# Optimization experiments

Measured on AMD Instinct MI355X. Metric: run time of the kernel, lower is better.

The kernel has to match this reference:

```python
import jax, jax.numpy as jnp
import numpy as np

HIDDEN = 2048
NUM_HEADS = 16
HEAD_DIM = HIDDEN // NUM_HEADS


def setup_inputs() -> dict:
    key = jax.random.key(0)
    k1, k2, k3 = jax.random.split(key, 3)
    B, S = 2, 2048
    hidden_states = jax.random.normal(k1, (B, S, HIDDEN), dtype=jnp.float32)
    attention_mask = jnp.zeros((B, 1, 1, S), dtype=jnp.float32)
    W_qkv = jax.random.normal(k2, (HIDDEN, 3 * HIDDEN), dtype=jnp.float32) * (1.0 / np.sqrt(HIDDEN))
    b_qkv = jnp.zeros((3 * HIDDEN,), dtype=jnp.float32)
    W_out = jax.random.normal(k3, (HIDDEN, HIDDEN), dtype=jnp.float32) * (1.0 / np.sqrt(HIDDEN))
    b_out = jnp.zeros((HIDDEN,), dtype=jnp.float32)
    return {"hidden_states": hidden_states, "attention_mask": attention_mask,
            "W_qkv": W_qkv, "b_qkv": b_qkv, "W_out": W_out, "b_out": b_out}


def reference(hidden_states, attention_mask, W_qkv, b_qkv, W_out, b_out):
    B, S, H = hidden_states.shape
    scale = 1.0 / np.sqrt(HEAD_DIM)
    # fused QKV projection (column-parallel linear, world_size=1)
    mixed = hidden_states @ W_qkv + b_qkv                      # [B,S,3H]
    q, k, v = jnp.split(mixed, 3, axis=-1)
    # [B, heads, S, head_dim]
    q = q.reshape(B, S, NUM_HEADS, HEAD_DIM).transpose(0, 2, 1, 3)
    k = k.reshape(B, S, NUM_HEADS, HEAD_DIM).transpose(0, 2, 1, 3)
    v = v.reshape(B, S, NUM_HEADS, HEAD_DIM).transpose(0, 2, 1, 3)
    scores = jnp.einsum('bhqd,bhkd->bhqk', q, k) * scale       # [B,h,S,S]
    scores = scores + attention_mask                            # additive mask broadcast
    probs = jax.nn.softmax(scores, axis=-1)
    ctx = jnp.einsum('bhqk,bhkd->bhqd', probs, v)               # [B,h,S,d]
    ctx = ctx.transpose(0, 2, 1, 3).reshape(B, S, H)
    return ctx @ W_out + b_out
```

## Files before the change

### kernel.cpp

```cpp
#include <hip/hip_runtime.h>
#include <hip/hip_bf16.h>
#include <stdint.h>

typedef __attribute__((ext_vector_type(4))) float   f32x4;
typedef __attribute__((ext_vector_type(8))) __bf16  bf16x8;
typedef __attribute__((ext_vector_type(4))) __bf16  bf16x4;
typedef __attribute__((ext_vector_type(8))) short   s16x8;
typedef __attribute__((ext_vector_type(4))) unsigned short u16x4;
typedef __attribute__((ext_vector_type(4))) float   fl4;

#define DEVFN static __device__ __forceinline__

constexpr int BATCH = 2, SEQ = 2048, HID = 2048, NHEAD = 16, HDIM = 128;
constexpr int MROWS = BATCH * SEQ;
constexpr int N3    = 3 * HID;
constexpr float ATT_SCALE = 0.08838834764831845f;
constexpr float LOG2E = 1.44269504088896340736f;

DEVFN unsigned short f2bf(float f) {
  unsigned int u = __float_as_uint(f);
  u += 0x7FFFu + ((u >> 16) & 1u);
  return (unsigned short)(u >> 16);
}
DEVFN float bf2f(unsigned short h) { return __uint_as_float(((unsigned int)h) << 16); }

DEVFN void async_cp16(const void* g, void* l) {
  __builtin_amdgcn_global_load_lds(
      (__attribute__((address_space(1))) void*)g,
      (__attribute__((address_space(3))) void*)l, 16, 0, 0);
}

DEVFN f32x4 mfma_bf16(bf16x8 a, bf16x8 b, f32x4 c) {
  return __builtin_amdgcn_mfma_f32_16x16x32_bf16(a, b, c, 0, 0, 0);
}

__global__ __launch_bounds__(256) void cvt_bf16(const float* __restrict__ x,
                                                unsigned short* __restrict__ hi, int n4) {
  for (int i = blockIdx.x * blockDim.x + threadIdx.x; i < n4; i += gridDim.x * blockDim.x) {
    fl4 v = ((const fl4*)x)[i];
    u16x4 h;
#pragma unroll
    for (int j = 0; j < 4; j++) h[j] = f2bf(v[j]);
    ((u16x4*)hi)[i] = h;
  }
}

__global__ __launch_bounds__(256) void cvt_transpose(const float* __restrict__ W,
                                                     unsigned short* __restrict__ T,
                                                     int R, int C) {
  __shared__ float tile[32][33];
  const int c0 = blockIdx.x * 32, r0 = blockIdx.y * 32;
  const int tx = threadIdx.x, ty = threadIdx.y;
#pragma unroll
  for (int i = 0; i < 4; i++) tile[ty + 8 * i][tx] = W[(size_t)(r0 + ty + 8 * i) * C + c0 + tx];
  __syncthreads();
#pragma unroll
  for (int i = 0; i < 4; i++) {
    const float v = tile[tx][ty + 8 * i];
    T[(size_t)(c0 + ty + 8 * i) * R + r0 + tx] = f2bf(v);
  }
}

template <bool OUT_BF16>
__global__ __launch_bounds__(256) void gemm_bt(const unsigned short* __restrict__ A,
                                               const unsigned short* __restrict__ Bt,
                                               const float* __restrict__ bias,
                                               void* __restrict__ Cout, int Ndim, int Kdim) {
  __shared__ __align__(16) unsigned short smem[2 * 128 * 64];
  unsigned short* sA = smem;
  unsigned short* sB = smem + 128 * 64;

  const int tid = threadIdx.x;
  const int wid = tid >> 6, lane = tid & 63;
  const int wm = wid >> 1, wn = wid & 1;
  const int g = lane >> 4, q = lane & 15;
  const int n0 = blockIdx.x * 128, m0 = blockIdx.y * 128;
  const int lrow = lane >> 3, lcolB = (lane & 7) << 4;

  f32x4 acc[4][4] = {};

  for (int k0 = 0; k0 < Kdim; k0 += 64) {
    __syncthreads();
#pragma unroll
    for (int i = 0; i < 4; i++) {
      const int trow = (wid << 5) + (i << 3) + lrow;
      const int scol = lcolB ^ ((trow & 7) << 4);
      const int dstB = ((wid << 5) + (i << 3)) << 7;
      async_cp16((const char*)A  + (((size_t)(m0 + trow) * Kdim + k0) << 1) + scol, (char*)sA + dstB);
      async_cp16((const char*)Bt + (((size_t)(n0 + trow) * Kdim + k0) << 1) + scol, (char*)sB + dstB);
    }
    __syncthreads();
#pragma unroll
    for (int kk = 0; kk < 2; kk++) {
      const int kbyte = (kk << 6) + (g << 4);
      bf16x8 a_h[4], b_h[4];
#pragma unroll
      for (int mf = 0; mf < 4; mf++) {
        const int row = (wm << 6) + (mf << 4) + q;
        a_h[mf] = *(const bf16x8*)((const char*)sA + (row << 7) + (kbyte ^ ((row & 7) << 4)));
      }
#pragma unroll
      for (int nf = 0; nf < 4; nf++) {
        const int row = (wn << 6) + (nf << 4) + q;
        b_h[nf] = *(const bf16x8*)((const char*)sB + (row << 7) + (kbyte ^ ((row & 7) << 4)));
      }
#pragma unroll
      for (int mf = 0; mf < 4; mf++)
#pragma unroll
        for (int nf = 0; nf < 4; nf++)
          acc[mf][nf] = mfma_bf16(a_h[mf], b_h[nf], acc[mf][nf]);
    }
  }

  float bv[4];
#pragma unroll
  for (int nf = 0; nf < 4; nf++) bv[nf] = bias[n0 + (wn << 6) + (nf << 4) + q];
#pragma unroll
  for (int mf = 0; mf < 4; mf++) {
    const int rowg = m0 + (wm << 6) + (mf << 4) + (g << 2);
#pragma unroll
    for (int nf = 0; nf < 4; nf++) {
      const int colg = n0 + (wn << 6) + (nf << 4) + q;
#pragma unroll
      for (int r = 0; r < 4; r++) {
        const float v = acc[mf][nf][r] + bv[nf];
        if (OUT_BF16)
          ((unsigned short*)Cout)[(size_t)(rowg + r) * Ndim + colg] = f2bf(v);
        else
          ((float*)Cout)[(size_t)(rowg + r) * Ndim + colg] = v;
      }
    }
  }
}

__global__ __launch_bounds__(256) void transpose_v(const unsigned short* __restrict__ qkv,
                                                   unsigned short* __restrict__ vt) {
  __shared__ __align__(16) unsigned short tile[64][136];
  const int z = blockIdx.y, b = z >> 4, h = z & 15;
  const int s0 = blockIdx.x << 6;
  const int t = threadIdx.x;
#pragma unroll
  for (int i = 0; i < 4; i++) {
    const int idx = t + (i << 8);
    const int row = idx >> 4, ch = idx & 15;
    *(s16x8*)&tile[row][ch << 3] =
        *(const s16x8*)(qkv + (size_t)(b * SEQ + s0 + row) * N3 + 2 * HID + h * HDIM + (ch << 3));
  }
  __syncthreads();
#pragma unroll
  for (int i = 0; i < 4; i++) {
    const int idx = t + (i << 8);
    const int d = idx >> 3, sc = idx & 7;
    s16x8 v;
#pragma unroll
    for (int j = 0; j < 8; j++) v[j] = (short)tile[(sc << 3) + j][d];
    *(s16x8*)(vt + (size_t)(z * HDIM + d) * SEQ + s0 + (sc << 3)) = v;
  }
}

__global__ __launch_bounds__(256, 2) void attn_kernel(const unsigned short* __restrict__ qkv,
                                                      const unsigned short* __restrict__ vt,
                                                      const float* __restrict__ mask,
                                                      unsigned short* __restrict__ ctx) {
  __shared__ __align__(16) unsigned short sK[64 * 128];
  __shared__ __align__(16) unsigned short sV[128 * 64];
  __shared__ __align__(16) unsigned short sP[4][32 * 72];

  const int z = blockIdx.y, b = z >> 4, h = z & 15;
  const int qb = blockIdx.x;
  const int tid = threadIdx.x, wid = tid >> 6, lane = tid & 63;
  const int g = lane >> 4, q = lane & 15;
  const int q0 = (qb << 7) + (wid << 5);

  bf16x8 bq[2][4];
#pragma unroll
  for (int qs = 0; qs < 2; qs++) {
    const unsigned short* qrow = qkv + (size_t)(b * SEQ + q0 + (qs << 4) + q) * N3 + h * HDIM;
#pragma unroll
    for (int c = 0; c < 4; c++) bq[qs][c] = *(const bf16x8*)(qrow + (c << 5) + (g << 3));
  }

  f32x4 acc[2][8] = {};
  float mrun[2] = {-1e30f, -1e30f}, lrun[2] = {0.f, 0.f};
  const int lrow8 = lane >> 3, lcol8 = (lane & 7) << 4;
  const int lrow16 = lane >> 4, lcol16 = (lane & 15) << 4;
  unsigned short* myP = &sP[wid][0];
  const int sbase = (lane & 48) | (g << 2);

  for (int k0 = 0; k0 < SEQ; k0 += 64) {
    __syncthreads();
#pragma unroll
    for (int i = 0; i < 4; i++) {
      const int kr = (wid << 4) + (i << 2) + lrow16;
      const int kcol = lcol16 ^ ((kr & 7) << 4);
      async_cp16((const char*)qkv + (((size_t)(b * SEQ + k0 + kr) * N3 + HID + h * HDIM) << 1) + kcol,
                 (char*)sK + (((wid << 4) + (i << 2)) << 8));
      const int vr = (wid << 5) + (i << 3) + lrow8;
      const int vcol = lcol8 ^ ((vr & 7) << 4);
      async_cp16((const char*)vt + (((size_t)(z * HDIM + vr) * SEQ + k0) << 1) + vcol,
                 (char*)sV + (((wid << 5) + (i << 3)) << 7));
    }
    __syncthreads();

    f32x4 accs[2][4];
#pragma unroll
    for (int qs = 0; qs < 2; qs++)
#pragma unroll
      for (int kt = 0; kt < 4; kt++) accs[qs][kt] = (f32x4){0.f, 0.f, 0.f, 0.f};
#pragma unroll
    for (int c = 0; c < 4; c++) {
      const int kbyte = (c << 6) + (g << 4);
#pragma unroll
      for (int kt = 0; kt < 4; kt++) {
        const int key = (kt << 4) + q;
        const bf16x8 ak = *(const bf16x8*)((const char*)sK + (key << 8) + (kbyte ^ ((key & 7) << 4)));
        accs[0][kt] = mfma_bf16(ak, bq[0][c], accs[0][kt]);
        accs[1][kt] = mfma_bf16(ak, bq[1][c], accs[1][kt]);
      }
    }

#pragma unroll
    for (int qs = 0; qs < 2; qs++) {
      float sv[4][4];
      float mt = -1e30f;
#pragma unroll
      for (int kt = 0; kt < 4; kt++) {
        const fl4 mk = *(const fl4*)(mask + (size_t)b * SEQ + k0 + (kt << 4) + (g << 2));
#pragma unroll
        for (int r = 0; r < 4; r++) {
          const float s = accs[qs][kt][r] * ATT_SCALE + mk[r];
          sv[kt][r] = s;
          mt = fmaxf(mt, s);
        }
      }
      mt = fmaxf(mt, __shfl_xor(mt, 16));
      mt = fmaxf(mt, __shfl_xor(mt, 32));
      if (!__all(mt <= mrun[qs] + 8.f)) {
        const float mnew = fmaxf(mrun[qs], mt);
        const float fs = exp2f((mrun[qs] - mnew) * LOG2E);
        lrun[qs] *= fs;
#pragma unroll
        for (int r = 0; r < 4; r++) {
          const float fr = __shfl(fs, sbase + r);
#pragma unroll
          for (int dt = 0; dt < 8; dt++) acc[qs][dt][r] *= fr;
        }
        mrun[qs] = mnew;
      }
      float ps = 0.f;
#pragma unroll
      for (int kt = 0; kt < 4; kt++) {
        bf16x4 pk;
#pragma unroll
        for (int r = 0; r < 4; r++) {
          const float e = exp2f((sv[kt][r] - mrun[qs]) * LOG2E);
          ps += e;
          pk[r] = (__bf16)e;
        }
        *(bf16x4*)((char*)myP + ((qs << 4) + q) * 144 + (((kt << 4) + (g << 2)) << 1)) = pk;
      }
      ps += __shfl_xor(ps, 16);
      ps += __shfl_xor(ps, 32);
      lrun[qs] += ps;
    }

    asm volatile("s_waitcnt lgkmcnt(0)" ::: "memory");
    __builtin_amdgcn_sched_barrier(0);

#pragma unroll
    for (int kc = 0; kc < 2; kc++) {
      const bf16x8 pa0 = *(const bf16x8*)((const char*)myP + q * 144 + (kc << 6) + (g << 4));
      const bf16x8 pa1 = *(const bf16x8*)((const char*)myP + (16 + q) * 144 + (kc << 6) + (g << 4));
      const int kbyte = (kc << 6) + (g << 4);
#pragma unroll
      for (int dt = 0; dt < 8; dt++) {
        const int d = (dt << 4) + q;
        const bf16x8 bvv = *(const bf16x8*)((const char*)sV + (d << 7) + (kbyte ^ ((d & 7) << 4)));
        acc[0][dt] = mfma_bf16(pa0, bvv, acc[0][dt]);
        acc[1][dt] = mfma_bf16(pa1, bvv, acc[1][dt]);
      }
    }
  }

#pragma unroll
  for (int qs = 0; qs < 2; qs++)
#pragma unroll
    for (int r = 0; r < 4; r++) {
      const float lr = __shfl(lrun[qs], sbase + r);
      const float inv = 1.f / lr;
      const int token = b * SEQ + (qb << 7) + (wid << 5) + (qs << 4) + (g << 2) + r;
      unsigned short* crow = ctx + (size_t)token * HID + h * HDIM + q;
#pragma unroll
      for (int dt = 0; dt < 8; dt++) crow[dt << 4] = f2bf(acc[qs][dt][r] * inv);
    }
}

extern "C" void kernel_launch(void* const* d_in, const int* in_sizes, int n_in,
                              void* d_out, int out_size, void* d_ws, size_t ws_size,
                              hipStream_t stream) {
  const float* hs   = (const float*)d_in[0];
  const float* mask = (const float*)d_in[1];
  const float* Wqkv = (const float*)d_in[2];
  const float* bqkv = (const float*)d_in[3];
  const float* Wout = (const float*)d_in[4];
  const float* bout = (const float*)d_in[5];

  char* ws = (char*)d_ws;
  size_t off = 0;
  auto alloc = [&](size_t n) { char* p = ws + off; off += (n + 255) & ~(size_t)255; return p; };
  unsigned short* hs_bf = (unsigned short*)alloc((size_t)MROWS * HID * 2);
  unsigned short* wq_bf = (unsigned short*)alloc((size_t)N3 * HID * 2);
  unsigned short* wo_bf = (unsigned short*)alloc((size_t)HID * HID * 2);
  unsigned short* qkvb  = (unsigned short*)alloc((size_t)MROWS * N3 * 2);
  unsigned short* vtb   = (unsigned short*)alloc((size_t)BATCH * NHEAD * HDIM * SEQ * 2);
  unsigned short* ctxb  = (unsigned short*)alloc((size_t)MROWS * HID * 2);
  (void)ws_size;

  cvt_bf16<<<2048, 256, 0, stream>>>(hs, hs_bf, MROWS * HID / 4);
  dim3 tb(32, 8);
  cvt_transpose<<<dim3(N3 / 32, HID / 32), tb, 0, stream>>>(Wqkv, wq_bf, HID, N3);
  cvt_transpose<<<dim3(HID / 32, HID / 32), tb, 0, stream>>>(Wout, wo_bf, HID, HID);
  gemm_bt<true ><<<dim3(N3 / 128, MROWS / 128), 256, 0, stream>>>(hs_bf, wq_bf, bqkv, qkvb, N3, HID);
  transpose_v<<<dim3(SEQ / 64, BATCH * NHEAD), 256, 0, stream>>>(qkvb, vtb);
  attn_kernel<<<dim3(SEQ / 128, BATCH * NHEAD), 256, 0, stream>>>(qkvb, vtb, mask, ctxb);
  gemm_bt<false><<<dim3(HID / 128, MROWS / 128), 256, 0, stream>>>(ctxb, wo_bf, bout, (float*)d_out, HID, HID);
}
```

Measured before the change: 305.2 us.

## Replace GEMM with triple-buffered async-copy ring and larger 256x128 tiles

Both projection GEMMs move to a new kernel with a 256x128 block tile, 512 threads and a three-slot shared-memory ring. Each step issues async global-to-LDS copies two tiles ahead and waits with explicit vmcnt counts before a single barrier, so loads overlap the MFMA work instead of stalling at two barriers per tile. The larger tile raises reuse per loaded byte but uses 144KB of LDS, which allows only one block per CU, and it hard-codes K=2048.

```diff
diff --git a/kernel.cpp b/kernel.cpp
--- a/kernel.cpp
+++ b/kernel.cpp
@@ -62,68 +62,104 @@
 }
 
 template <bool OUT_BF16>
-__global__ __launch_bounds__(256) void gemm_bt(const unsigned short* __restrict__ A,
-                                               const unsigned short* __restrict__ Bt,
-                                               const float* __restrict__ bias,
-                                               void* __restrict__ Cout, int Ndim, int Kdim) {
-  __shared__ __align__(16) unsigned short smem[2 * 128 * 64];
-  unsigned short* sA = smem;
-  unsigned short* sB = smem + 128 * 64;
+__global__ __launch_bounds__(512, 1) void gemm_ring(const unsigned short* __restrict__ A,
+                                                    const unsigned short* __restrict__ Bt,
+                                                    const float* __restrict__ bias,
+                                                    void* __restrict__ Cout, int Ndim) {
+  constexpr int KDIM  = 2048;
+  constexpr int NT    = KDIM / 64;
+  constexpr int ASLOT = 256 * 64;
+  constexpr int BSLOT = 128 * 64;
+  constexpr int SLOT  = ASLOT + BSLOT;
+  __shared__ __align__(16) unsigned short smem[3 * SLOT];
 
   const int tid = threadIdx.x;
   const int wid = tid >> 6, lane = tid & 63;
-  const int wm = wid >> 1, wn = wid & 1;
+  const int wm = wid >> 2, wn = wid & 3;
   const int g = lane >> 4, q = lane & 15;
-  const int n0 = blockIdx.x * 128, m0 = blockIdx.y * 128;
-  const int lrow = lane >> 3, lcolB = (lane & 7) << 4;
-
-  f32x4 acc[4][4] = {};
-
-  for (int k0 = 0; k0 < Kdim; k0 += 64) {
-    __syncthreads();
-#pragma unroll
-    for (int i = 0; i < 4; i++) {
-      const int trow = (wid << 5) + (i << 3) + lrow;
-      const int scol = lcolB ^ ((trow & 7) << 4);
-      const int dstB = ((wid << 5) + (i << 3)) << 7;
-      async_cp16((const char*)A  + (((size_t)(m0 + trow) * Kdim + k0) << 1) + scol, (char*)sA + dstB);
-      async_cp16((const char*)Bt + (((size_t)(n0 + trow) * Kdim + k0) << 1) + scol, (char*)sB + dstB);
-    }
-    __syncthreads();
-#pragma unroll
-    for (int kk = 0; kk < 2; kk++) {
-      const int kbyte = (kk << 6) + (g << 4);
-      bf16x8 a_h[4], b_h[4];
-#pragma unroll
-      for (int mf = 0; mf < 4; mf++) {
-        const int row = (wm << 6) + (mf << 4) + q;
-        a_h[mf] = *(const bf16x8*)((const char*)sA + (row << 7) + (kbyte ^ ((row & 7) << 4)));
-      }
-#pragma unroll
-      for (int nf = 0; nf < 4; nf++) {
-        const int row = (wn << 6) + (nf << 4) + q;
-        b_h[nf] = *(const bf16x8*)((const char*)sB + (row << 7) + (kbyte ^ ((row & 7) << 4)));
-      }
-#pragma unroll
-      for (int mf = 0; mf < 4; mf++)
-#pragma unroll
-        for (int nf = 0; nf < 4; nf++)
-          acc[mf][nf] = mfma_bf16(a_h[mf], b_h[nf], acc[mf][nf]);
-    }
-  }
-
-  float bv[4];
-#pragma unroll
-  for (int nf = 0; nf < 4; nf++) bv[nf] = bias[n0 + (wn << 6) + (nf << 4) + q];
-#pragma unroll
-  for (int mf = 0; mf < 4; mf++) {
-    const int rowg = m0 + (wm << 6) + (mf << 4) + (g << 2);
-#pragma unroll
-    for (int nf = 0; nf < 4; nf++) {
-      const int colg = n0 + (wn << 6) + (nf << 4) + q;
+  const int n0 = blockIdx.x * 128, m0 = blockIdx.y * 256;
+
+  const int srow = (wid << 3) + (lane >> 3);
+  const int scol = (((lane & 7) ^ (lane >> 3)) << 4);
+  const char* gA = (const char*)A  + ((size_t)(m0 + srow) * KDIM) * 2 + scol;
+  const char* gB = (const char*)Bt + ((size_t)(n0 + srow) * KDIM) * 2 + scol;
+  const int dbase = ((wid << 3)) << 7;
+
+  f32x4 acc[8][2] = {};
+  const int axor = (q & 7) << 4;
+
+  auto STAGE = [&](int tt, int slot) {
+    char* sA = (char*)(smem + slot * SLOT);
+    char* sB = (char*)(smem + slot * SLOT + ASLOT);
+    const size_t koff = (size_t)tt << 7;
+#pragma unroll
+    for (int i = 0; i < 4; i++)
+      async_cp16(gA + (size_t)(i * 64) * (KDIM * 2) + koff, sA + dbase + (i << 13));
+#pragma unroll
+    for (int i = 0; i < 2; i++)
+      async_cp16(gB + (size_t)(i * 64) * (KDIM * 2) + koff, sB + dbase + (i << 13));
+  };
+
+  auto COMPUTE = [&](int slot) {
+    const char* sA = (const char*)(smem + slot * SLOT);
+    const char* sB = (const char*)(smem + slot * SLOT + ASLOT);
+#pragma unroll
+    for (int ks = 0; ks < 2; ks++) {
+      const int kb = (ks << 6) + (g << 4);
+      bf16x8 av[8], bv[2];
+#pragma unroll
+      for (int nf = 0; nf < 2; nf++) {
+        const int row = (wn << 5) + (nf << 4) + q;
+        bv[nf] = *(const bf16x8*)(sB + (row << 7) + (kb ^ axor));
+      }
+#pragma unroll
+      for (int mf = 0; mf < 8; mf++) {
+        const int row = (wm << 7) + (mf << 4) + q;
+        av[mf] = *(const bf16x8*)(sA + (row << 7) + (kb ^ axor));
+      }
+#pragma unroll
+      for (int mf = 0; mf < 8; mf++)
+#pragma unroll
+        for (int nf = 0; nf < 2; nf++)
+          acc[mf][nf] = mfma_bf16(av[mf], bv[nf], acc[mf][nf]);
+    }
+  };
+
+  STAGE(0, 0);
+  STAGE(1, 1);
+  int s2 = 2, sc = 0;
+#pragma unroll 1
+  for (int t = 0; t < NT - 2; ++t) {
+    asm volatile("s_waitcnt vmcnt(6)" ::: "memory");
+    __builtin_amdgcn_s_barrier();
+    asm volatile("" ::: "memory");
+    STAGE(t + 2, s2);
+    COMPUTE(sc);
+    s2 = (s2 == 2) ? 0 : s2 + 1;
+    sc = (sc == 2) ? 0 : sc + 1;
+  }
+  asm volatile("s_waitcnt vmcnt(6)" ::: "memory");
+  __builtin_amdgcn_s_barrier();
+  asm volatile("" ::: "memory");
+  COMPUTE(sc);
+  sc = (sc == 2) ? 0 : sc + 1;
+  asm volatile("s_waitcnt vmcnt(0)" ::: "memory");
+  __builtin_amdgcn_s_barrier();
+  asm volatile("" ::: "memory");
+  COMPUTE(sc);
+
+  float bvv[2];
+#pragma unroll
+  for (int nf = 0; nf < 2; nf++) bvv[nf] = bias[n0 + (wn << 5) + (nf << 4) + q];
+#pragma unroll
+  for (int mf = 0; mf < 8; mf++) {
+    const int rowg = m0 + (wm << 7) + (mf << 4) + (g << 2);
+#pragma unroll
+    for (int nf = 0; nf < 2; nf++) {
+      const int colg = n0 + (wn << 5) + (nf << 4) + q;
 #pragma unroll
       for (int r = 0; r < 4; r++) {
-        const float v = acc[mf][nf][r] + bv[nf];
+        const float v = acc[mf][nf][r] + bvv[nf];
         if (OUT_BF16)
           ((unsigned short*)Cout)[(size_t)(rowg + r) * Ndim + colg] = f2bf(v);
         else
@@ -320,8 +356,8 @@
   dim3 tb(32, 8);
   cvt_transpose<<<dim3(N3 / 32, HID / 32), tb, 0, stream>>>(Wqkv, wq_bf, HID, N3);
   cvt_transpose<<<dim3(HID / 32, HID / 32), tb, 0, stream>>>(Wout, wo_bf, HID, HID);
-  gemm_bt<true ><<<dim3(N3 / 128, MROWS / 128), 256, 0, stream>>>(hs_bf, wq_bf, bqkv, qkvb, N3, HID);
+  gemm_ring<true ><<<dim3(N3 / 128, MROWS / 256), 512, 0, stream>>>(hs_bf, wq_bf, bqkv, qkvb, N3);
   transpose_v<<<dim3(SEQ / 64, BATCH * NHEAD), 256, 0, stream>>>(qkvb, vtb);
   attn_kernel<<<dim3(SEQ / 128, BATCH * NHEAD), 256, 0, stream>>>(qkvb, vtb, mask, ctxb);
-  gemm_bt<false><<<dim3(HID / 128, MROWS / 128), 256, 0, stream>>>(ctxb, wo_bf, bout, (float*)d_out, HID, HID);
-}
+  gemm_ring<false><<<dim3(HID / 128, MROWS / 256), 512, 0, stream>>>(ctxb, wo_bf, bout, (float*)d_out, HID);
+}
```

After: 278.0 us. -8.9%, faster.
